# Kernel tuning notes

Measured on AMD Instinct MI355X. Metric: run time of the kernel, lower is better.

The kernel has to match this reference:

```python
import jax, jax.numpy as jnp
import numpy as np

EPS = 1e-15  # 0.1 ** 15 in the original


def _mi_table(T):
    # Mutual information of a joint-probability table T [nx, ny]
    P_x = jnp.sum(T, axis=1)  # [nx]
    P_y = jnp.sum(T, axis=0)  # [ny]
    T_xy = P_x[:, None] * P_y[None, :]  # outer product [nx, ny]
    mi = jnp.sum(T * (jnp.log((T + EPS) / (T_xy + EPS)) / jnp.log(jnp.float32(2.0))))
    return mi


def setup_inputs() -> dict:
    key = jax.random.key(0)
    k1, k2 = jax.random.split(key)
    N_ins, N_att, K = 16384, 8192, 64
    Ur = jax.random.uniform(k1, (N_ins, K), dtype=jnp.float32)
    Uc = jax.random.uniform(k2, (N_att, K), dtype=jnp.float32)
    return {"Ur": Ur, "Uc": Uc, "nclu_row": K, "nclu_col": K}


def reference(Ur, Uc, nclu_row, nclu_col):
    # joint probability table  [N_ins, N_att]
    T = Ur @ Uc.T
    T = T / jnp.sum(T)

    v1 = jnp.argmax(Ur, axis=1)  # hard row-cluster ids  [N_ins]
    v2 = jnp.argmax(Uc, axis=1)  # hard col-cluster ids  [N_att]

    # Reduce_Table: segment-sum rows then columns (replaces looped mask+concat)
    T_r = jax.ops.segment_sum(T, v1, num_segments=nclu_row)          # [nclu_row, N_att]
    T_rr = jax.ops.segment_sum(T_r.T, v2, num_segments=nclu_col).T  # [nclu_row, nclu_col]

    mi_org = _mi_table(T)
    mi_red = _mi_table(T_rr)

    loss = jnp.log(1.0 + jnp.abs(1.0 - mi_red / mi_org))
    return loss
```

## Files before the change

### kernel.cpp

```cpp
#include <hip/hip_runtime.h>
#include <hip/hip_bf16.h>

#define N_INS 16384
#define N_ATT 8192
#define KDIM  64

typedef __attribute__((ext_vector_type(8))) short bf16x8;
typedef __attribute__((ext_vector_type(4))) float f32x4;

#define OFF_UCB    0
#define OFF_CPR    1048576
#define OFF_CPC    1064960
#define OFF_ASEG   1073152
#define OFF_BSEG   1089536
#define OFF_GACC   1105920
#define OFF_TK     1106688

#define NBLK_SEG   96
#define NBLK_U     96
#define NBLK_HEAVY 2048
#define NBLK_K2    (NBLK_SEG + NBLK_U + NBLK_HEAVY)

__device__ __forceinline__ unsigned short f2bf(float x) {
    unsigned u = __float_as_uint(x);
    u = (u + 0x7FFFu + ((u >> 16) & 1u)) >> 16;
    return (unsigned short)u;
}

__device__ __forceinline__ float wave_red(float v) {
#pragma unroll
    for (int o = 32; o > 0; o >>= 1) v += __shfl_down(v, o, 64);
    return v;
}

typedef __attribute__((address_space(3))) unsigned int as3_u32;
typedef const __attribute__((address_space(1))) unsigned int as1_u32;
__device__ __forceinline__ void stage16(void* l, const void* g) {
    __builtin_amdgcn_global_load_lds((as1_u32*)g, (as3_u32*)l, 16, 0, 0);
}

__global__ __launch_bounds__(256)
void k_prep(const float* __restrict__ Ur, const float* __restrict__ Uc,
            float* __restrict__ cpr, float* __restrict__ cpc,
            unsigned short* __restrict__ Ucb,
            float* __restrict__ Aseg, float* __restrict__ Bseg,
            double* __restrict__ Gacc, unsigned* __restrict__ tickets) {
    __shared__ float cs2[256];
    int blk = blockIdx.x, tid = threadIdx.x;
    if (blk < 128) {
        int gid = blk * 256 + tid;
        for (int c = gid; c < N_ATT * 8; c += 32768) {
            int t = c >> 7, o = c & 127;
            int q, m;
            if (o < 64) { q = o >> 4; m = o & 15; }
            else        { q = 4 + ((o - 64) >> 4); m = (o - 64) & 15; }
            int r = t * 16 + m;
            const float4* src = (const float4*)(Uc + (size_t)r * 64 + q * 8);
            float4 x0 = src[0], x1 = src[1];
            uint4 v;
            v.x = (unsigned)f2bf(x0.x) | ((unsigned)f2bf(x0.y) << 16);
            v.y = (unsigned)f2bf(x0.z) | ((unsigned)f2bf(x0.w) << 16);
            v.z = (unsigned)f2bf(x1.x) | ((unsigned)f2bf(x1.y) << 16);
            v.w = (unsigned)f2bf(x1.z) | ((unsigned)f2bf(x1.w) << 16);
            *(uint4*)((unsigned char*)Ucb + (size_t)c * 16) = v;
        }
        return;
    }
    if (blk == 224) {
        float4 z4 = {0.f, 0.f, 0.f, 0.f};
        for (int i = tid; i < 1024; i += 256) ((float4*)Aseg)[i] = z4;
        for (int i = tid; i < 1024; i += 256) ((float4*)Bseg)[i] = z4;
        if (tid < 96) Gacc[tid] = 0.0;
        if (tid < 64) { tickets[tid] = 0u; tickets[64 + tid] = 0u;
                        tickets[128 + tid] = 0u; tickets[192 + tid] = 0u; }
        if (tid < 16) tickets[256 + tid] = 0u;
        return;
    }
    bool isUr = blk < 192;
    int b = isUr ? (blk - 128) : (blk - 192);
    const float* base = (isUr ? Ur : Uc) + (size_t)b * 256 * KDIM;
    float* dst = (isUr ? cpr : cpc) + b * 64;
    int col = tid & 63, r0 = tid >> 6;
    float s = 0.f;
    for (int r = r0; r < 256; r += 4) s += base[r * KDIM + col];
    cs2[tid] = s;
    __syncthreads();
    if (tid < 64) dst[tid] = cs2[tid] + cs2[tid + 64] + cs2[tid + 128] + cs2[tid + 192];
}

__global__ __launch_bounds__(256)
void k_main(const float* __restrict__ Ur, const float* __restrict__ Uc,
            const unsigned char* __restrict__ Ucb,
            const float* __restrict__ cpr, const float* __restrict__ cpc,
            float* __restrict__ Aseg, float* __restrict__ Bseg,
            double* __restrict__ Gacc, unsigned* __restrict__ tickets,
            float* __restrict__ out) {
    __shared__ __align__(16) unsigned char smem[17408];
    __shared__ int flagS;
    int tid = threadIdx.x, blk = blockIdx.x;
    int wvi = tid >> 6, lane = tid & 63;

    if (blk < NBLK_SEG) {
        float* Part = (float*)smem;
        int*   bins = (int*)(smem + 16384);
        bool isUr = blk < 64;
        int b = isUr ? blk : (blk - 64);
        const float* M = isUr ? Ur : Uc;
        float* Seg = isUr ? Aseg : Bseg;
        int base_row = b * 256;
        for (int i = tid; i < 4096; i += 256) Part[i] = 0.f;
        __syncthreads();
        {
            const float* rp = M + (size_t)(base_row + tid) * KDIM;
            float best = -1e30f; int bidx = 0;
#pragma unroll
            for (int k = 0; k < 64; k += 4) {
                float4 v = *(const float4*)(rp + k);
                if (v.x > best) { best = v.x; bidx = k; }
                if (v.y > best) { best = v.y; bidx = k + 1; }
                if (v.z > best) { best = v.z; bidx = k + 2; }
                if (v.w > best) { best = v.w; bidx = k + 3; }
            }
            bins[tid] = bidx;
        }
        __syncthreads();
        {
            int r0 = wvi * 64;
            const float* Mb = M + (size_t)(base_row + r0) * 64 + lane;
#pragma unroll 4
            for (int r = 0; r < 64; ++r) {
                int bb = bins[r0 + r];
                float val = Mb[(size_t)r * 64];
                atomicAdd(&Part[bb * 64 + lane], val);
            }
        }
        __syncthreads();
        for (int i = tid; i < 4096; i += 256)
            atomicAdd(&Seg[i], Part[i]);
    } else if (blk < NBLK_SEG + NBLK_U) {
        float* wv = (float*)smem;
        bool isUr = blk < (NBLK_SEG + 64);
        int b = isUr ? (blk - NBLK_SEG) : (blk - NBLK_SEG - 64);
        const float* M = isUr ? Ur : Uc;
        int base_row = b * 256;
        if (tid < 64) {
            const float* cpw = isUr ? cpc : cpr;
            int nbw = isUr ? 32 : 64;
            float s = 0.f;
            for (int p = 0; p < nbw; ++p) s += cpw[p * 64 + tid];
            wv[tid] = s;
        }
        __syncthreads();
        const float* rp = M + (size_t)(base_row + tid) * KDIM;
        float u = 0.f;
#pragma unroll
        for (int k = 0; k < 64; k += 4) {
            float4 v = *(const float4*)(rp + k);
            u += v.x * wv[k] + v.y * wv[k + 1] + v.z * wv[k + 2] + v.w * wv[k + 3];
        }
        float pw = wave_red(u * __log2f(u));
        if (lane == 0)
            atomicAdd(&Gacc[(isUr ? 64 : 80) + (b & 15)], (double)pw);
    } else {
        unsigned char* bufs = smem;
        float* gshW = (float*)(smem + 16384);
        int hb = blk - NBLK_SEG - NBLK_U;
        int quad = lane >> 4, m = lane & 15;
        int rb = hb & 127, cc = hb >> 7;
        int row0 = rb * 128 + wvi * 32;
        bf16x8 a[2][2];
#pragma unroll
        for (int t = 0; t < 2; ++t) {
            int ridx = row0 + t * 16 + m;
            const float* rp = Ur + (size_t)ridx * 64 + quad * 8;
#pragma unroll
            for (int h = 0; h < 2; ++h) {
                const float* rph = rp + h * 32;
                float4 x0 = *(const float4*)rph;
                float4 x1 = *(const float4*)(rph + 4);
                bf16x8 f;
                f[0] = (short)f2bf(x0.x); f[1] = (short)f2bf(x0.y);
                f[2] = (short)f2bf(x0.z); f[3] = (short)f2bf(x0.w);
                f[4] = (short)f2bf(x1.x); f[5] = (short)f2bf(x1.y);
                f[6] = (short)f2bf(x1.z); f[7] = (short)f2bf(x1.w);
                a[t][h] = f;
            }
        }
        const unsigned char* gB = Ucb + (size_t)(cc * 32) * 2048;
        int soff = wvi * 2048 + lane * 16;
        stage16(bufs + soff, gB + soff);
        stage16(bufs + soff + 1024, gB + soff + 1024);
        int loff = lane * 16;
        float g = 0.f;
#pragma unroll 1
        for (int pg = 0; pg < 8; ++pg) {
            __syncthreads();
            if (pg < 7) {
                const unsigned char* gn = gB + (size_t)(pg + 1) * 8192;
                unsigned char* bn = bufs + (((pg + 1) & 1) << 13);
                stage16(bn + soff, gn + soff);
                stage16(bn + soff + 1024, gn + soff + 1024);
            }
            const unsigned char* bg = bufs + ((pg & 1) << 13);
#pragma unroll
            for (int p = 0; p < 2; ++p) {
                const unsigned char* bb = bg + p * 4096;
                bf16x8 c00 = *(const bf16x8*)(bb + loff);
                bf16x8 c01 = *(const bf16x8*)(bb + 1024 + loff);
                bf16x8 c10 = *(const bf16x8*)(bb + 2048 + loff);
                bf16x8 c11 = *(const bf16x8*)(bb + 3072 + loff);
                f32x4 acc00 = {0.f,0.f,0.f,0.f}, acc01 = {0.f,0.f,0.f,0.f};
                f32x4 acc10 = {0.f,0.f,0.f,0.f}, acc11 = {0.f,0.f,0.f,0.f};
                acc00 = __builtin_amdgcn_mfma_f32_16x16x32_bf16(a[0][0], c00, acc00, 0, 0, 0);
                acc00 = __builtin_amdgcn_mfma_f32_16x16x32_bf16(a[0][1], c01, acc00, 0, 0, 0);
                acc10 = __builtin_amdgcn_mfma_f32_16x16x32_bf16(a[1][0], c00, acc10, 0, 0, 0);
                acc10 = __builtin_amdgcn_mfma_f32_16x16x32_bf16(a[1][1], c01, acc10, 0, 0, 0);
                acc01 = __builtin_amdgcn_mfma_f32_16x16x32_bf16(a[0][0], c10, acc01, 0, 0, 0);
                acc01 = __builtin_amdgcn_mfma_f32_16x16x32_bf16(a[0][1], c11, acc01, 0, 0, 0);
                acc11 = __builtin_amdgcn_mfma_f32_16x16x32_bf16(a[1][0], c10, acc11, 0, 0, 0);
                acc11 = __builtin_amdgcn_mfma_f32_16x16x32_bf16(a[1][1], c11, acc11, 0, 0, 0);
#pragma unroll
                for (int e = 0; e < 4; ++e) {
                    float d0 = acc00[e]; g += d0 * __log2f(d0);
                    float d1 = acc01[e]; g += d1 * __log2f(d1);
                    float d2 = acc10[e]; g += d2 * __log2f(d2);
                    float d3 = acc11[e]; g += d3 * __log2f(d3);
                }
            }
        }
        float gw = wave_red(g);
        if (lane == 0) gshW[wvi] = gw;
        __syncthreads();
        if (tid == 0) {
            float gs = gshW[0] + gshW[1] + gshW[2] + gshW[3];
            atomicAdd(&Gacc[hb & 63], (double)gs);
        }
    }

    __builtin_amdgcn_s_waitcnt(0);
    __syncthreads();
    if (tid == 0) {
        flagS = 0;
        unsigned old = atomicAdd(&tickets[(blk & 15) << 4], 1u);
        if (old == (NBLK_K2 / 16) - 1) {
            unsigned old2 = atomicAdd(&tickets[256], 1u);
            flagS = (old2 == 15u);
        }
    }
    __syncthreads();
    if (!flagS) return;

    float*  Prx = (float*)smem;
    float*  Pry = (float*)(smem + 256);
    double* sc  = (double*)(smem + 512);
    double* red = (double*)(smem + 1024);
    if (tid < 64) {
        double sa = 0.0, sb = 0.0;
        for (int p = 0; p < 64; ++p) sa += (double)cpr[p * 64 + tid];
        for (int p = 0; p < 32; ++p) sb += (double)cpc[p * 64 + tid];
        red[tid] = sa * sb;
        Prx[tid] = 0.f; Pry[tid] = 0.f;
    }
    __syncthreads();
    if (tid == 0) {
        double s = 0.0;
        for (int k = 0; k < 64; ++k) s += red[k];
        sc[0] = s;
        double gg = 0.0;
        for (int k = 0; k < 64; ++k) gg += Gacc[k];
        sc[1] = gg;
    } else if (tid == 1) {
        double s = 0.0;
        for (int k = 64; k < 80; ++k) s += Gacc[k];
        sc[2] = s;
    } else if (tid == 2) {
        double s = 0.0;
        for (int k = 80; k < 96; ++k) s += Gacc[k];
        sc[3] = s;
    }
    __syncthreads();
    double S = sc[0];
    int p = tid >> 2, q0 = (tid & 3) * 16;
    float tloc[16];
    {
        float prow_sum = 0.f;
        for (int qi = 0; qi < 16; ++qi) {
            int q = q0 + qi;
            double s = 0.0;
            for (int k = 0; k < 64; ++k)
                s += (double)Aseg[p * 64 + k] * (double)Bseg[q * 64 + k];
            float t = (float)(s / S);
            tloc[qi] = t;
            prow_sum += t;
            atomicAdd(&Pry[q], t);
        }
        atomicAdd(&Prx[p], prow_sum);
    }
    __syncthreads();
    {
        const double EPSd = 1e-15;
        double part = 0.0;
        for (int qi = 0; qi < 16; ++qi) {
            double t = (double)tloc[qi];
            double txy = (double)Prx[p] * (double)Pry[q0 + qi];
            part += t * log((t + EPSd) / (txy + EPSd));
        }
        red[tid] = part;
    }
    __syncthreads();
    for (int s2 = 128; s2 > 0; s2 >>= 1) {
        if (tid < s2) red[tid] += red[tid + s2];
        __syncthreads();
    }
    if (tid == 0) {
        const double inv_ln2 = 1.4426950408889634;
        double mi_red = red[0] * inv_ln2;
        double G = sc[1], Uu = sc[2], Vv = sc[3];
        double log2S = log(S) * inv_ln2;
        double mi_org = G / S + log2S - (Uu + Vv) / S;
        double loss = log(1.0 + fabs(1.0 - mi_red / mi_org));
        out[0] = (float)loss;
    }
}

extern "C" void kernel_launch(void* const* d_in, const int* in_sizes, int n_in,
                              void* d_out, int out_size, void* d_ws, size_t ws_size,
                              hipStream_t stream) {
    const float* Ur = (const float*)d_in[0];
    const float* Uc = (const float*)d_in[1];
    float* out = (float*)d_out;
    char* ws = (char*)d_ws;
    unsigned short* Ucb = (unsigned short*)(ws + OFF_UCB);
    float* cpr   = (float*)(ws + OFF_CPR);
    float* cpc   = (float*)(ws + OFF_CPC);
    float* Aseg  = (float*)(ws + OFF_ASEG);
    float* Bseg  = (float*)(ws + OFF_BSEG);
    double* Gacc = (double*)(ws + OFF_GACC);
    unsigned* tickets = (unsigned*)(ws + OFF_TK);

    k_prep<<<225, 256, 0, stream>>>(Ur, Uc, cpr, cpc, Ucb, Aseg, Bseg, Gacc, tickets);
    k_main<<<NBLK_K2, 256, 0, stream>>>(Ur, Uc, (const unsigned char*)Ucb,
                                        cpr, cpc, Aseg, Bseg, Gacc, tickets, out);
}
```

Measured before the change: 161.9 us.

## Replace contended global atomics in segment-sum with per-block partials and last-block reduction

Each segment-sum block now writes its 4096-entry partial table to a workspace buffer instead of atomically adding into the shared Aseg/Bseg tables. A ticket counter picks the last finishing block, which sums all 96 partials and writes the totals. This removes heavy atomic contention on the same 8K addresses, but it serializes a 96x4096 reduction onto a single block, which may lengthen the critical path if the downstream heavy blocks wait on Aseg/Bseg.

```diff
diff --git a/kernel.cpp b/kernel.cpp
--- a/kernel.cpp
+++ b/kernel.cpp
@@ -15,6 +15,7 @@
 #define OFF_BSEG   1089536
 #define OFF_GACC   1105920
 #define OFF_TK     1106688
+#define OFF_SEGP   1108096
 
 #define NBLK_SEG   96
 #define NBLK_U     96
@@ -71,9 +72,8 @@
         for (int i = tid; i < 1024; i += 256) ((float4*)Aseg)[i] = z4;
         for (int i = tid; i < 1024; i += 256) ((float4*)Bseg)[i] = z4;
         if (tid < 96) Gacc[tid] = 0.0;
-        if (tid < 64) { tickets[tid] = 0u; tickets[64 + tid] = 0u;
-                        tickets[128 + tid] = 0u; tickets[192 + tid] = 0u; }
-        if (tid < 16) tickets[256 + tid] = 0u;
+        if (tid < 96) { tickets[tid] = 0u; tickets[96 + tid] = 0u; }
+        if (tid < 96) tickets[192 + tid] = 0u;
         return;
     }
     bool isUr = blk < 192;
@@ -93,6 +93,7 @@
             const unsigned char* __restrict__ Ucb,
             const float* __restrict__ cpr, const float* __restrict__ cpc,
             float* __restrict__ Aseg, float* __restrict__ Bseg,
+            float* __restrict__ segparts,
             double* __restrict__ Gacc, unsigned* __restrict__ tickets,
             float* __restrict__ out) {
     __shared__ __align__(16) unsigned char smem[17408];
@@ -106,7 +107,6 @@
         bool isUr = blk < 64;
         int b = isUr ? blk : (blk - 64);
         const float* M = isUr ? Ur : Uc;
-        float* Seg = isUr ? Aseg : Bseg;
         int base_row = b * 256;
         for (int i = tid; i < 4096; i += 256) Part[i] = 0.f;
         __syncthreads();
@@ -135,8 +135,25 @@
             }
         }
         __syncthreads();
-        for (int i = tid; i < 4096; i += 256)
-            atomicAdd(&Seg[i], Part[i]);
+        float* sp = segparts + (size_t)blk * 4096;
+        for (int i = tid; i < 4096; i += 256) sp[i] = Part[i];
+        __threadfence();
+        __syncthreads();
+        if (tid == 0) {
+            unsigned old = atomicAdd(&tickets[272], 1u);
+            flagS = (old == NBLK_SEG - 1);
+        }
+        __syncthreads();
+        if (flagS) {
+            for (int j = tid; j < 4096; j += 256) {
+                float sa = 0.f;
+                for (int p = 0; p < 64; ++p)  sa += segparts[(size_t)p * 4096 + j];
+                atomicAdd(&Aseg[j], sa);
+                float sb = 0.f;
+                for (int p = 64; p < 96; ++p) sb += segparts[(size_t)p * 4096 + j];
+                atomicAdd(&Bseg[j], sb);
+            }
+        }
     } else if (blk < NBLK_SEG + NBLK_U) {
         float* wv = (float*)smem;
         bool isUr = blk < (NBLK_SEG + 64);
@@ -337,8 +354,10 @@
     float* Bseg  = (float*)(ws + OFF_BSEG);
     double* Gacc = (double*)(ws + OFF_GACC);
     unsigned* tickets = (unsigned*)(ws + OFF_TK);
+    float* segparts = (float*)(ws + OFF_SEGP);
 
     k_prep<<<225, 256, 0, stream>>>(Ur, Uc, cpr, cpc, Ucb, Aseg, Bseg, Gacc, tickets);
     k_main<<<NBLK_K2, 256, 0, stream>>>(Ur, Uc, (const unsigned char*)Ucb,
-                                        cpr, cpc, Aseg, Bseg, Gacc, tickets, out);
-}
+                                        cpr, cpc, Aseg, Bseg, segparts,
+                                        Gacc, tickets, out);
+}
```

New measurement: 226.8 us. +40.1%, slower.
